# Kernel tuning notes

Hardware: AMD Instinct MI355X
Metric: run time of the kernel (lower is better)

## Reference

```python
import jax, jax.numpy as jnp
import numpy as np


def _propagate(x, src, dst, norm, n):
    # PyG propagate with aggr='add': out[dst_e] += norm_e * x[src_e]
    return jax.ops.segment_sum(x[src] * norm[:, None], dst, num_segments=n)


def _dconv(x, w, b, row, col, norm_out, norm_in, n):
    # DConv with K=2: w has shape (2, 2, c_in, c_out)
    # k=0 term: identity for both diffusion directions
    h = x @ w[0, 0] + x @ w[1, 0]
    # k=1 term: 1-hop diffusion, forward edges and flipped edges
    tx_o = _propagate(x, row, col, norm_out, n)  # out-degree normalized walk
    tx_i = _propagate(x, col, row, norm_in, n)   # edge_index.flip([0]) walk
    h = h + tx_o @ w[0, 1] + tx_i @ w[1, 1]
    return h + b


def reference(x, edge_index, edge_weight, w_lin2, b_lin2, w_z, b_z, w_r, b_r, w_h, b_h, w_out, b_out):
    n = x.shape[0]
    row, col = edge_index[0], edge_index[1]
    # degrees from weighted adjacency (same as to_dense_adj row/col sums)
    deg_out = jax.ops.segment_sum(edge_weight, row, num_segments=n)
    deg_in = jax.ops.segment_sum(edge_weight, col, num_segments=n)
    norm_out = (1.0 / deg_out)[row]
    norm_in = (1.0 / deg_in)[row]

    h = x.reshape(n, -1)                      # Flatten: (n, 24)
    h = jax.nn.sigmoid(h @ w_lin2 + b_lin2)   # (n, hidden)

    # DCRNN GRU cell, hidden state initialized to zeros (single step)
    h0 = jnp.zeros_like(h)
    xh = jnp.concatenate([h, h0], axis=1)     # (n, 2*hidden)
    z = jax.nn.sigmoid(_dconv(xh, w_z, b_z, row, col, norm_out, norm_in, n))
    r = jax.nn.sigmoid(_dconv(xh, w_r, b_r, row, col, norm_out, norm_in, n))
    xhr = jnp.concatenate([h, h0 * r], axis=1)
    h_tilde = jnp.tanh(_dconv(xhr, w_h, b_h, row, col, norm_out, norm_in, n))
    h_new = z * h0 + (1.0 - z) * h_tilde

    return jax.nn.sigmoid(h_new) @ w_out + b_out  # (n, out_periods)


def setup_inputs() -> dict:
    key = jax.random.key(0)
    ks = jax.random.split(key, 12)
    N, DEG, HID, OUTP, WIN, HOR = 100000, 8, 64, 12, 2, 12
    E = N * DEG

    x = jax.random.normal(ks[0], (N, WIN, HOR), dtype=jnp.float32)

    # random edges + a ring so every node has out-degree>=1 and in-degree>=1
    e_rand = N * (DEG - 1)
    row_r = jax.random.randint(ks[1], (e_rand,), 0, N, dtype=jnp.int32)
    col_r = jax.random.randint(ks[2], (e_rand,), 0, N, dtype=jnp.int32)
    ring = jnp.arange(N, dtype=jnp.int32)
    row = jnp.concatenate([row_r, ring])
    col = jnp.concatenate([col_r, (ring + 1) % N])
    edge_index = jnp.stack([row, col])  # (2, E)
    edge_weight = jax.random.uniform(ks[3], (E,), minval=0.5, maxval=1.5, dtype=jnp.float32)

    def lin_w(k, fi, fo):
        return jax.random.normal(k, (fi, fo), jnp.float32) / np.float32(np.sqrt(fi))

    def dconv_w(k, cin, cout):
        return jax.random.normal(k, (2, 2, cin, cout), jnp.float32) / np.float32(np.sqrt(cin))

    cin = 2 * HID
    return {
        "x": x,
        "edge_index": edge_index,
        "edge_weight": edge_weight,
        "w_lin2": lin_w(ks[4], WIN * HOR, HID),
        "b_lin2": jnp.zeros((HID,), jnp.float32),
        "w_z": dconv_w(ks[5], cin, HID),
        "b_z": jnp.zeros((HID,), jnp.float32),
        "w_r": dconv_w(ks[6], cin, HID),
        "b_r": jnp.zeros((HID,), jnp.float32),
        "w_h": dconv_w(ks[7], cin, HID),
        "b_h": jnp.zeros((HID,), jnp.float32),
        "w_out": lin_w(ks[8], HID, OUTP),
        "b_out": jnp.zeros((OUTP,), jnp.float32),
    }
```

## Files before the change

### kernel.cpp

```cpp
#include <hip/hip_runtime.h>


typedef unsigned long long ull;
typedef unsigned short ushort;
typedef unsigned int uint;
typedef __attribute__((ext_vector_type(8))) short bf16x8;
typedef __attribute__((ext_vector_type(4))) float f32x4;

#define BSZ    64
#define CAP    768
#define CHUNK  2048
#define MAXBKT 2048

__device__ __forceinline__ float sigmoid_f(float x) {
    return 1.0f / (1.0f + __expf(-x));
}
__device__ __forceinline__ float tanh_f(float x) {
    float ax = fabsf(x);
    float e = __expf(-2.0f * ax);
    float t = (1.0f - e) / (1.0f + e);
    return copysignf(t, x);
}
__device__ __forceinline__ ushort f2bf(float f) {
    unsigned u = __float_as_uint(f);
    return (ushort)((u + 0x7FFF + ((u >> 16) & 1)) >> 16);
}

__global__ void __launch_bounds__(256) mega1_kernel(
        const int* __restrict__ row, const int* __restrict__ col,
        const float* __restrict__ ew, int E,
        uint* __restrict__ gcur, uint* __restrict__ pkbuf,
        int nbkt, int nslot,
        const float* __restrict__ x, const float* __restrict__ Wl,
        const float* __restrict__ bl, ushort* __restrict__ hb, int N,
        const float* __restrict__ wz, const float* __restrict__ bz,
        const float* __restrict__ wh, const float* __restrict__ bh,
        ushort* __restrict__ Wp, float* __restrict__ bc, int SB, int LB) {
    __shared__ uint smem[MAXBKT];
    int bx = blockIdx.x;
    const int t = threadIdx.x;

    if (bx < SB) {
        uint* hist = smem;
        const int d  = bx & 1;
        const int e0 = (bx >> 1) * CHUNK;
        const int* key = d ? row : col;
        const int* oth = d ? col : row;
        for (int i = t; i < nbkt; i += 256) hist[i] = 0;
        __syncthreads();
#pragma unroll
        for (int j = 0; j < CHUNK / 256; ++j) {
            int e = e0 + j * 256 + t;
            if (e < E) atomicAdd(&hist[key[e] >> 6], 1u);
        }
        __syncthreads();
        for (int i = t; i < nbkt; i += 256) {
            uint c = hist[i];
            hist[i] = c ? (uint)i * CAP + atomicAdd(&gcur[d * nbkt + i], c) : 0u;
        }
        __syncthreads();
#pragma unroll
        for (int j = 0; j < CHUNK / 256; ++j) {
            int e = e0 + j * 256 + t;
            if (e < E) {
                int k   = key[e];
                int bkt = k >> 6;
                uint w9 = (uint)(ew[e] * 256.0f + 0.5f);
                uint s = atomicAdd(&hist[bkt], 1u);
                if (s < ((uint)bkt + 1u) * CAP)
                    pkbuf[(size_t)d * nslot + s] =
                        ((uint)oth[e] << 15) |
                        ((uint)(k & (BSZ - 1)) << 9) | w9;
            }
        }
        return;
    }
    bx -= SB;
    if (bx < LB) {
        float* Ws = (float*)smem;
        float* bs = Ws + 24 * 64;
        for (int i = t; i < 384; i += 256)
            ((float4*)Ws)[i] = ((const float4*)Wl)[i];
        if (t < 64) bs[t] = bl[t];
        __syncthreads();
        const int c = t & 63;
        const int w = t >> 6;
        const int n0 = bx * 16 + w * 4;
#pragma unroll
        for (int q = 0; q < 4; ++q) {
            int n = n0 + q;
            if (n >= N) break;
            const float* xr = x + (size_t)n * 24;
            float acc = bs[c];
#pragma unroll
            for (int k4 = 0; k4 < 6; ++k4) {
                float4 xv = *(const float4*)(xr + k4 * 4);
                acc = fmaf(xv.x, Ws[(k4 * 4 + 0) * 64 + c], acc);
                acc = fmaf(xv.y, Ws[(k4 * 4 + 1) * 64 + c], acc);
                acc = fmaf(xv.z, Ws[(k4 * 4 + 2) * 64 + c], acc);
                acc = fmaf(xv.w, Ws[(k4 * 4 + 3) * 64 + c], acc);
            }
            hb[(size_t)n * 64 + c] = f2bf(sigmoid_f(acc));
        }
        return;
    }
    bx -= LB;
    int i = bx * 256 + t;
    if (bx == 0 && t < 128) bc[t] = (t < 64) ? bz[t] : bh[t - 64];
    if (i >= 6 * 8 * 64 * 8) return;
    int j    = i & 7;
    int lane = (i >> 3) & 63;
    int ct   = (i >> 9) & 7;
    int kt   = i >> 12;
    int k = kt * 32 + 8 * (lane >> 4) + j;
    int c = ct * 16 + (lane & 15);
    const float* w = (c < 64) ? wz : wh;
    int cc = c & 63;
    float v;
    if (k < 64)        v = w[(0 * 128 + k) * 64 + cc] + w[(2 * 128 + k) * 64 + cc];
    else if (k < 128)  v = w[(1 * 128 + (k - 64)) * 64 + cc];
    else               v = w[(3 * 128 + (k - 128)) * 64 + cc];
    Wp[i] = f2bf(v);
}

__global__ void __launch_bounds__(256) sort_kernel(
        const uint* __restrict__ gcur, const uint* __restrict__ pkbuf,
        uint* __restrict__ srt, int2* __restrict__ be,
        float* __restrict__ rdi, float* __restrict__ rdo,
        int nbkt, int nslot, int N) {
    __shared__ uint hist[BSZ];
    __shared__ uint cur[BSZ];
    __shared__ float sdeg[BSZ];
    const int b = blockIdx.x, d = blockIdx.y, t = threadIdx.x;
    if (t < BSZ) { hist[t] = 0; sdeg[t] = 0.0f; }
    __syncthreads();
    uint cnt = gcur[d * nbkt + b];
    if (cnt > CAP) cnt = CAP;
    const uint* rec = pkbuf + (size_t)d * nslot + (size_t)b * CAP;
    for (uint i = t; i < cnt; i += 256) {
        uint r = rec[i];
        uint dl = (r >> 9) & (BSZ - 1);
        atomicAdd(&hist[dl], 1u);
        atomicAdd(&sdeg[dl], (float)(r & 0x1FFu));
    }
    __syncthreads();
    if (t < BSZ) {
        int v = (int)hist[t];
        int x = v;
#pragma unroll
        for (int off = 1; off < BSZ; off <<= 1) {
            int y = __shfl_up(x, off, 64);
            if (t >= off) x += y;
        }
        uint p = (uint)(x - v);
        cur[t] = p;
        int n = b * BSZ + t;
        if (n < N) {
            be[(size_t)d * N + n] =
                make_int2((int)((uint)b * CAP + p),
                          (int)((uint)b * CAP + p + (uint)v));
            float s = sdeg[t];
            float rv = (s > 0.0f) ? (256.0f / s) : 0.0f;
            if (d == 0) rdi[n] = rv;
            else        rdo[n] = rv;
        }
    }
    __syncthreads();
    uint* so = srt + (size_t)d * nslot + (size_t)b * CAP;
    for (uint i = t; i < cnt; i += 256) {
        uint r = rec[i];
        uint dl = (r >> 9) & (BSZ - 1);
        uint p = atomicAdd(&cur[dl], 1u);
        so[p] = r >> 15;
    }
}

__global__ void __launch_bounds__(256) gather_kernel(
        const ushort* __restrict__ hb, const uint* __restrict__ srt,
        const int2* __restrict__ be,
        const float* __restrict__ rdo, const float* __restrict__ rdi,
        ushort* __restrict__ pob, ushort* __restrict__ pib,
        int nslot, int N) {
    const int lane = threadIdx.x & 63;
    const int g    = lane >> 4;
    const int cq   = (lane & 15) * 4;
    const int d    = blockIdx.y;
    const uint* s_  = srt + (size_t)d * nslot;
    const int2* be_ = be + (size_t)d * N;

    int wid  = blockIdx.x * 4 + (threadIdx.x >> 6);
    int step = gridDim.x * 4;
    if (wid >= N) return;

    int2 r0 = be_[wid];
    uint ia = s_[min(r0.x + g,     r0.y - 1)];
    uint ib = s_[min(r0.x + 4 + g, r0.y - 1)];

    for (int n = wid; n < N; n += step) {
        int nn = n + step;
        bool has_next = (nn < N);
        int2 r1 = r0;
        if (has_next) r1 = be_[nn];

        float a0 = 0.f, a1 = 0.f, a2 = 0.f, a3 = 0.f;
        int s = r0.x, e = r0.y;
        while (s < e) {
            int sn = s + 8;
            uint ia_n = ia, ib_n = ib;
            if (sn < e) {
                ia_n = s_[min(sn + g,     e - 1)];
                ib_n = s_[min(sn + 4 + g, e - 1)];
            } else if (has_next) {
                ia_n = s_[min(r1.x + g,     r1.y - 1)];
                ib_n = s_[min(r1.x + 4 + g, r1.y - 1)];
            }
            bool va = (s + g < e), vb = (s + 4 + g < e);
            float wa, wb;
            if (d == 0) {
                wa = va ? rdo[ia] : 0.0f;
                wb = vb ? rdo[ib] : 0.0f;
            } else {
                wa = va ? 1.0f : 0.0f;
                wb = vb ? 1.0f : 0.0f;
            }
            uint2 ha = *(const uint2*)(hb + (size_t)ia * 64 + cq);
            uint2 hc = *(const uint2*)(hb + (size_t)ib * 64 + cq);
            a0 = fmaf(__uint_as_float(ha.x << 16),         wa, a0);
            a1 = fmaf(__uint_as_float(ha.x & 0xFFFF0000u), wa, a1);
            a2 = fmaf(__uint_as_float(ha.y << 16),         wa, a2);
            a3 = fmaf(__uint_as_float(ha.y & 0xFFFF0000u), wa, a3);
            a0 = fmaf(__uint_as_float(hc.x << 16),         wb, a0);
            a1 = fmaf(__uint_as_float(hc.x & 0xFFFF0000u), wb, a1);
            a2 = fmaf(__uint_as_float(hc.y << 16),         wb, a2);
            a3 = fmaf(__uint_as_float(hc.y & 0xFFFF0000u), wb, a3);
            s = sn; ia = ia_n; ib = ib_n;
        }
        a0 += __shfl_xor(a0, 16, 64); a0 += __shfl_xor(a0, 32, 64);
        a1 += __shfl_xor(a1, 16, 64); a1 += __shfl_xor(a1, 32, 64);
        a2 += __shfl_xor(a2, 16, 64); a2 += __shfl_xor(a2, 32, 64);
        a3 += __shfl_xor(a3, 16, 64); a3 += __shfl_xor(a3, 32, 64);

        if (lane < 16) {
            float m = (d == 0) ? 1.0f : rdi[n];
            uint lo = (uint)f2bf(a0 * m) | ((uint)f2bf(a1 * m) << 16);
            uint hi = (uint)f2bf(a2 * m) | ((uint)f2bf(a3 * m) << 16);
            ushort* dst = (d == 0 ? pob : pib) + (size_t)n * 64 + cq;
            *(uint2*)dst = make_uint2(lo, hi);
        }
        r0 = r1;
    }
}

__global__ void __launch_bounds__(256) gates_kernel(
        const ushort* __restrict__ hb, const ushort* __restrict__ pob,
        const ushort* __restrict__ pib, const ushort* __restrict__ Wp,
        const float* __restrict__ bc, const float* __restrict__ wout,
        const float* __restrict__ bout, float* __restrict__ out, int N) {
    __shared__ float sS[64 * 68];
    __shared__ float sWO[64 * 12];
    const int t    = threadIdx.x;
    const int w    = t >> 6;
    const int lane = t & 63;
    const int n0   = blockIdx.x * 64;

    for (int i = t; i < 64 * 12; i += 256) sWO[i] = wout[i];

    f32x4 acc[8];
#pragma unroll
    for (int ct = 0; ct < 8; ++ct) {
        float bcv = bc[ct * 16 + (lane & 15)];
        acc[ct] = (f32x4){bcv, bcv, bcv, bcv};
    }

    int arow = n0 + w * 16 + (lane & 15);
    if (arow >= N) arow = N - 1;
    const int g8 = (lane >> 4) * 8;
    const ushort* const srcs[3] = {hb, pob, pib};

#pragma unroll
    for (int kc = 0; kc < 6; ++kc) {
        const ushort* src = srcs[kc >> 1];
        bf16x8 a = *(const bf16x8*)(src + (size_t)arow * 64 + (kc & 1) * 32 + g8);
#pragma unroll
        for (int ct = 0; ct < 8; ++ct) {
            bf16x8 b = *(const bf16x8*)(Wp + (size_t)((kc * 8 + ct) * 64 + lane) * 8);
            acc[ct] = __builtin_amdgcn_mfma_f32_16x16x32_bf16(a, b, acc[ct], 0, 0, 0);
        }
    }

    const int rowbase = w * 16 + (lane >> 4) * 4;
    const int colbase = lane & 15;
#pragma unroll
    for (int ct = 0; ct < 4; ++ct) {
#pragma unroll
        for (int r = 0; r < 4; ++r) {
            float zv = sigmoid_f(acc[ct][r]);
            float ht = tanh_f(acc[ct + 4][r]);
            sS[(rowbase + r) * 68 + ct * 16 + colbase] =
                sigmoid_f((1.0f - zv) * ht);
        }
    }
    __syncthreads();

#pragma unroll
    for (int rr = 0; rr < 3; ++rr) {
        int o = rr * 256 + t;
        int node = o / 12;
        int j = o % 12;
        int n = n0 + node;
        if (n >= N) continue;
        float a = bout[j];
#pragma unroll 8
        for (int c2 = 0; c2 < 64; ++c2) a = fmaf(sS[node * 68 + c2], sWO[c2 * 12 + j], a);
        out[(size_t)n * 12 + j] = a;
    }
}

extern "C" void kernel_launch(void* const* d_in, const int* in_sizes, int n_in,
                              void* d_out, int out_size, void* d_ws, size_t ws_size,
                              hipStream_t stream) {
    const float* x      = (const float*)d_in[0];
    const int*   ei     = (const int*)  d_in[1];
    const float* ew     = (const float*)d_in[2];
    const float* w_lin2 = (const float*)d_in[3];
    const float* b_lin2 = (const float*)d_in[4];
    const float* w_z    = (const float*)d_in[5];
    const float* b_z    = (const float*)d_in[6];
    const float* w_h    = (const float*)d_in[9];
    const float* b_h    = (const float*)d_in[10];
    const float* w_out  = (const float*)d_in[11];
    const float* b_out  = (const float*)d_in[12];

    int N = in_sizes[0] / 24;
    int E = in_sizes[1] / 2;
    const int* row = ei;
    const int* col = ei + E;
    int nbkt  = (N + BSZ - 1) / BSZ;
    int nslot = nbkt * CAP;

    uint*   pkbuf = (uint*)d_ws;
    uint*   srt   = pkbuf + 2 * (size_t)nslot;
    ushort* hb    = (ushort*)(srt + 2 * (size_t)nslot);
    ushort* pob   = hb  + (size_t)N * 64;
    ushort* pib   = pob + (size_t)N * 64;
    ushort* Wp    = pib + (size_t)N * 64;
    float*  bc    = (float*)(Wp + 24576);
    float*  rdo   = bc + 128;
    float*  rdi   = rdo + N;
    int2*   be    = (int2*)(rdi + N);
    uint*   gcur  = (uint*)(be + 2 * (size_t)N);

    int SB = 2 * ((E + CHUNK - 1) / CHUNK);
    int LB = (N + 15) / 16;
    int PB = (6 * 8 * 64 * 8 + 255) / 256;

    hipMemsetAsync(gcur, 0, 2 * (size_t)nbkt * sizeof(uint), stream);
    mega1_kernel<<<SB + LB + PB, 256, 0, stream>>>(
        row, col, ew, E, gcur, pkbuf, nbkt, nslot,
        x, w_lin2, b_lin2, hb, N,
        w_z, b_z, w_h, b_h, Wp, bc, SB, LB);
    sort_kernel<<<dim3(nbkt, 2), 256, 0, stream>>>(gcur, pkbuf, srt, be,
                                                   rdi, rdo, nbkt, nslot, N);
    gather_kernel<<<dim3(2048, 2), 256, 0, stream>>>(hb, srt, be, rdo, rdi,
                                                     pob, pib, nslot, N);
    gates_kernel<<<(N + 63) / 64, 256, 0, stream>>>(hb, pob, pib, Wp, bc,
                                                    w_out, b_out, (float*)d_out, N);
}
```

Baseline: 151.9 us.

## Fuse bucket sort, neighbor gather and gate GEMM into one per-bucket kernel

Merges the sort, gather and gates kernels into a single kernel that processes one 64-node bucket per block. Sorted edge lists and the propagated features are kept in shared memory instead of being written to and read back from global buffers. A small separate kernel computes the out-degree normalization first, because the gather needs it for source nodes that belong to other buckets. In exchange, each block gathers its own nodes without the prefetch pipelining or the grid-stride load balancing of the old gather kernel, and uses more shared memory per block, which may reduce occupancy.

```diff
diff --git a/kernel.cpp b/kernel.cpp
--- a/kernel.cpp
+++ b/kernel.cpp
@@ -123,171 +123,158 @@
     Wp[i] = f2bf(v);
 }
 
-__global__ void __launch_bounds__(256) sort_kernel(
+__global__ void __launch_bounds__(256) deg1_kernel(
         const uint* __restrict__ gcur, const uint* __restrict__ pkbuf,
-        uint* __restrict__ srt, int2* __restrict__ be,
-        float* __restrict__ rdi, float* __restrict__ rdo,
-        int nbkt, int nslot, int N) {
-    __shared__ uint hist[BSZ];
-    __shared__ uint cur[BSZ];
+        float* __restrict__ rdo, int nbkt, int nslot, int N) {
     __shared__ float sdeg[BSZ];
-    const int b = blockIdx.x, d = blockIdx.y, t = threadIdx.x;
-    if (t < BSZ) { hist[t] = 0; sdeg[t] = 0.0f; }
-    __syncthreads();
-    uint cnt = gcur[d * nbkt + b];
+    const int b = blockIdx.x, t = threadIdx.x;
+    if (t < BSZ) sdeg[t] = 0.0f;
+    __syncthreads();
+    uint cnt = gcur[nbkt + b];
     if (cnt > CAP) cnt = CAP;
-    const uint* rec = pkbuf + (size_t)d * nslot + (size_t)b * CAP;
-    for (uint i = t; i < cnt; i += 256) {
-        uint r = rec[i];
-        uint dl = (r >> 9) & (BSZ - 1);
-        atomicAdd(&hist[dl], 1u);
-        atomicAdd(&sdeg[dl], (float)(r & 0x1FFu));
-    }
+    const uint* rec = pkbuf + (size_t)nslot + (size_t)b * CAP;
+    for (uint i = t; i < cnt; i += 256)
+        atomicAdd(&sdeg[(rec[i] >> 9) & (BSZ - 1)], (float)(rec[i] & 0x1FFu));
     __syncthreads();
     if (t < BSZ) {
-        int v = (int)hist[t];
-        int x = v;
-#pragma unroll
-        for (int off = 1; off < BSZ; off <<= 1) {
-            int y = __shfl_up(x, off, 64);
-            if (t >= off) x += y;
-        }
-        uint p = (uint)(x - v);
-        cur[t] = p;
         int n = b * BSZ + t;
-        if (n < N) {
-            be[(size_t)d * N + n] =
-                make_int2((int)((uint)b * CAP + p),
-                          (int)((uint)b * CAP + p + (uint)v));
-            float s = sdeg[t];
-            float rv = (s > 0.0f) ? (256.0f / s) : 0.0f;
-            if (d == 0) rdi[n] = rv;
-            else        rdo[n] = rv;
-        }
-    }
-    __syncthreads();
-    uint* so = srt + (size_t)d * nslot + (size_t)b * CAP;
-    for (uint i = t; i < cnt; i += 256) {
-        uint r = rec[i];
-        uint dl = (r >> 9) & (BSZ - 1);
-        uint p = atomicAdd(&cur[dl], 1u);
-        so[p] = r >> 15;
-    }
-}
-
-__global__ void __launch_bounds__(256) gather_kernel(
-        const ushort* __restrict__ hb, const uint* __restrict__ srt,
-        const int2* __restrict__ be,
-        const float* __restrict__ rdo, const float* __restrict__ rdi,
-        ushort* __restrict__ pob, ushort* __restrict__ pib,
-        int nslot, int N) {
-    const int lane = threadIdx.x & 63;
-    const int g    = lane >> 4;
-    const int cq   = (lane & 15) * 4;
-    const int d    = blockIdx.y;
-    const uint* s_  = srt + (size_t)d * nslot;
-    const int2* be_ = be + (size_t)d * N;
-
-    int wid  = blockIdx.x * 4 + (threadIdx.x >> 6);
-    int step = gridDim.x * 4;
-    if (wid >= N) return;
-
-    int2 r0 = be_[wid];
-    uint ia = s_[min(r0.x + g,     r0.y - 1)];
-    uint ib = s_[min(r0.x + 4 + g, r0.y - 1)];
-
-    for (int n = wid; n < N; n += step) {
-        int nn = n + step;
-        bool has_next = (nn < N);
-        int2 r1 = r0;
-        if (has_next) r1 = be_[nn];
-
-        float a0 = 0.f, a1 = 0.f, a2 = 0.f, a3 = 0.f;
-        int s = r0.x, e = r0.y;
-        while (s < e) {
-            int sn = s + 8;
-            uint ia_n = ia, ib_n = ib;
-            if (sn < e) {
-                ia_n = s_[min(sn + g,     e - 1)];
-                ib_n = s_[min(sn + 4 + g, e - 1)];
-            } else if (has_next) {
-                ia_n = s_[min(r1.x + g,     r1.y - 1)];
-                ib_n = s_[min(r1.x + 4 + g, r1.y - 1)];
+        if (n < N) rdo[n] = (sdeg[t] > 0.0f) ? (256.0f / sdeg[t]) : 0.0f;
+    }
+}
+
+__global__ void __launch_bounds__(256) mega2_kernel(
+        const uint* __restrict__ gcur, const uint* __restrict__ pkbuf,
+        const ushort* __restrict__ hb, const float* __restrict__ rdo,
+        const ushort* __restrict__ Wp, const float* __restrict__ bc,
+        const float* __restrict__ wout, const float* __restrict__ bout,
+        float* __restrict__ out, int nbkt, int nslot, int N) {
+    __shared__ uint   srt[2][CAP];
+    __shared__ ushort pt[2][BSZ][72];
+    __shared__ uint   histL[BSZ], curL[BSZ];
+    __shared__ uint   begL[2][BSZ];
+    __shared__ ushort cntL[2][BSZ];
+    __shared__ float  sdeg[BSZ], rdi_l[BSZ];
+    __shared__ float  sWO[64 * 12];
+
+    const int b = blockIdx.x, t = threadIdx.x;
+    const int w = t >> 6, lane = t & 63;
+
+    for (int i = t; i < 64 * 12; i += 256) sWO[i] = wout[i];
+
+    for (int d = 0; d < 2; ++d) {
+        if (t < BSZ) { histL[t] = 0; sdeg[t] = 0.0f; }
+        __syncthreads();
+        uint cnt = gcur[d * nbkt + b];
+        if (cnt > CAP) cnt = CAP;
+        const uint* rec = pkbuf + (size_t)d * nslot + (size_t)b * CAP;
+        for (uint i = t; i < cnt; i += 256) {
+            uint r = rec[i];
+            uint dl = (r >> 9) & (BSZ - 1);
+            atomicAdd(&histL[dl], 1u);
+            atomicAdd(&sdeg[dl], (float)(r & 0x1FFu));
+        }
+        __syncthreads();
+        if (t < BSZ) {
+            int v = (int)histL[t];
+            int x = v;
+#pragma unroll
+            for (int off = 1; off < BSZ; off <<= 1) {
+                int y = __shfl_up(x, off, 64);
+                if (t >= off) x += y;
             }
-            bool va = (s + g < e), vb = (s + 4 + g < e);
-            float wa, wb;
-            if (d == 0) {
-                wa = va ? rdo[ia] : 0.0f;
-                wb = vb ? rdo[ib] : 0.0f;
-            } else {
-                wa = va ? 1.0f : 0.0f;
-                wb = vb ? 1.0f : 0.0f;
+            uint p = (uint)(x - v);
+            curL[t] = p;
+            begL[d][t] = p;
+            cntL[d][t] = (ushort)v;
+            if (d == 0) rdi_l[t] = (sdeg[t] > 0.0f) ? (256.0f / sdeg[t]) : 0.0f;
+        }
+        __syncthreads();
+        for (uint i = t; i < cnt; i += 256) {
+            uint r = rec[i];
+            uint dl = (r >> 9) & (BSZ - 1);
+            uint p = atomicAdd(&curL[dl], 1u);
+            srt[d][p] = r >> 15;
+        }
+        __syncthreads();
+    }
+
+    {
+        const int g  = lane >> 4;
+        const int cq = (lane & 15) * 4;
+        for (int d = 0; d < 2; ++d) {
+            for (int nl = w; nl < BSZ; nl += 4) {
+                int s0 = (int)begL[d][nl];
+                int s1 = s0 + (int)cntL[d][nl];
+                float a0 = 0.f, a1 = 0.f, a2 = 0.f, a3 = 0.f;
+                for (int s = s0; s < s1; s += 8) {
+                    int sa = s + g, sb = s + 4 + g;
+                    uint ia = srt[d][(sa < s1) ? sa : s1 - 1];
+                    uint ib = srt[d][(sb < s1) ? sb : s1 - 1];
+                    float wa, wb;
+                    if (d == 0) {
+                        wa = (sa < s1) ? rdo[ia] : 0.0f;
+                        wb = (sb < s1) ? rdo[ib] : 0.0f;
+                    } else {
+                        wa = (sa < s1) ? 1.0f : 0.0f;
+                        wb = (sb < s1) ? 1.0f : 0.0f;
+                    }
+                    uint2 ha = *(const uint2*)(hb + (size_t)ia * 64 + cq);
+                    uint2 hc = *(const uint2*)(hb + (size_t)ib * 64 + cq);
+                    a0 = fmaf(__uint_as_float(ha.x << 16),         wa, a0);
+                    a1 = fmaf(__uint_as_float(ha.x & 0xFFFF0000u), wa, a1);
+                    a2 = fmaf(__uint_as_float(ha.y << 16),         wa, a2);
+                    a3 = fmaf(__uint_as_float(ha.y & 0xFFFF0000u), wa, a3);
+                    a0 = fmaf(__uint_as_float(hc.x << 16),         wb, a0);
+                    a1 = fmaf(__uint_as_float(hc.x & 0xFFFF0000u), wb, a1);
+                    a2 = fmaf(__uint_as_float(hc.y << 16),         wb, a2);
+                    a3 = fmaf(__uint_as_float(hc.y & 0xFFFF0000u), wb, a3);
+                }
+                a0 += __shfl_xor(a0, 16, 64); a0 += __shfl_xor(a0, 32, 64);
+                a1 += __shfl_xor(a1, 16, 64); a1 += __shfl_xor(a1, 32, 64);
+                a2 += __shfl_xor(a2, 16, 64); a2 += __shfl_xor(a2, 32, 64);
+                a3 += __shfl_xor(a3, 16, 64); a3 += __shfl_xor(a3, 32, 64);
+                if (lane < 16) {
+                    float m = (d == 0) ? 1.0f : rdi_l[nl];
+                    uint lo = (uint)f2bf(a0 * m) | ((uint)f2bf(a1 * m) << 16);
+                    uint hi = (uint)f2bf(a2 * m) | ((uint)f2bf(a3 * m) << 16);
+                    *(uint2*)&pt[d][nl][cq] = make_uint2(lo, hi);
+                }
             }
-            uint2 ha = *(const uint2*)(hb + (size_t)ia * 64 + cq);
-            uint2 hc = *(const uint2*)(hb + (size_t)ib * 64 + cq);
-            a0 = fmaf(__uint_as_float(ha.x << 16),         wa, a0);
-            a1 = fmaf(__uint_as_float(ha.x & 0xFFFF0000u), wa, a1);
-            a2 = fmaf(__uint_as_float(ha.y << 16),         wa, a2);
-            a3 = fmaf(__uint_as_float(ha.y & 0xFFFF0000u), wa, a3);
-            a0 = fmaf(__uint_as_float(hc.x << 16),         wb, a0);
-            a1 = fmaf(__uint_as_float(hc.x & 0xFFFF0000u), wb, a1);
-            a2 = fmaf(__uint_as_float(hc.y << 16),         wb, a2);
-            a3 = fmaf(__uint_as_float(hc.y & 0xFFFF0000u), wb, a3);
-            s = sn; ia = ia_n; ib = ib_n;
-        }
-        a0 += __shfl_xor(a0, 16, 64); a0 += __shfl_xor(a0, 32, 64);
-        a1 += __shfl_xor(a1, 16, 64); a1 += __shfl_xor(a1, 32, 64);
-        a2 += __shfl_xor(a2, 16, 64); a2 += __shfl_xor(a2, 32, 64);
-        a3 += __shfl_xor(a3, 16, 64); a3 += __shfl_xor(a3, 32, 64);
-
-        if (lane < 16) {
-            float m = (d == 0) ? 1.0f : rdi[n];
-            uint lo = (uint)f2bf(a0 * m) | ((uint)f2bf(a1 * m) << 16);
-            uint hi = (uint)f2bf(a2 * m) | ((uint)f2bf(a3 * m) << 16);
-            ushort* dst = (d == 0 ? pob : pib) + (size_t)n * 64 + cq;
-            *(uint2*)dst = make_uint2(lo, hi);
-        }
-        r0 = r1;
-    }
-}
-
-__global__ void __launch_bounds__(256) gates_kernel(
-        const ushort* __restrict__ hb, const ushort* __restrict__ pob,
-        const ushort* __restrict__ pib, const ushort* __restrict__ Wp,
-        const float* __restrict__ bc, const float* __restrict__ wout,
-        const float* __restrict__ bout, float* __restrict__ out, int N) {
-    __shared__ float sS[64 * 68];
-    __shared__ float sWO[64 * 12];
-    const int t    = threadIdx.x;
-    const int w    = t >> 6;
-    const int lane = t & 63;
-    const int n0   = blockIdx.x * 64;
-
-    for (int i = t; i < 64 * 12; i += 256) sWO[i] = wout[i];
-
+        }
+    }
+    __syncthreads();
+
+    const int n0 = b * BSZ;
     f32x4 acc[8];
 #pragma unroll
     for (int ct = 0; ct < 8; ++ct) {
         float bcv = bc[ct * 16 + (lane & 15)];
         acc[ct] = (f32x4){bcv, bcv, bcv, bcv};
     }
-
     int arow = n0 + w * 16 + (lane & 15);
     if (arow >= N) arow = N - 1;
     const int g8 = (lane >> 4) * 8;
-    const ushort* const srcs[3] = {hb, pob, pib};
+    const int lrow = w * 16 + (lane & 15);
 
 #pragma unroll
     for (int kc = 0; kc < 6; ++kc) {
-        const ushort* src = srcs[kc >> 1];
-        bf16x8 a = *(const bf16x8*)(src + (size_t)arow * 64 + (kc & 1) * 32 + g8);
+        bf16x8 a;
+        if (kc < 2) {
+            a = *(const bf16x8*)(hb + (size_t)arow * 64 + kc * 32 + g8);
+        } else {
+            const int dd   = (kc - 2) >> 1;
+            const int koff = (kc & 1) * 32;
+            a = *(const bf16x8*)(&pt[dd][lrow][koff + g8]);
+        }
 #pragma unroll
         for (int ct = 0; ct < 8; ++ct) {
-            bf16x8 b = *(const bf16x8*)(Wp + (size_t)((kc * 8 + ct) * 64 + lane) * 8);
-            acc[ct] = __builtin_amdgcn_mfma_f32_16x16x32_bf16(a, b, acc[ct], 0, 0, 0);
-        }
-    }
-
+            bf16x8 bb = *(const bf16x8*)(Wp + (size_t)((kc * 8 + ct) * 64 + lane) * 8);
+            acc[ct] = __builtin_amdgcn_mfma_f32_16x16x32_bf16(a, bb, acc[ct], 0, 0, 0);
+        }
+    }
+
+    __syncthreads();
+    float* sS = (float*)&pt[0][0][0];
     const int rowbase = w * 16 + (lane >> 4) * 4;
     const int colbase = lane & 15;
 #pragma unroll
@@ -311,7 +298,8 @@
         if (n >= N) continue;
         float a = bout[j];
 #pragma unroll 8
-        for (int c2 = 0; c2 < 64; ++c2) a = fmaf(sS[node * 68 + c2], sWO[c2 * 12 + j], a);
+        for (int c2 = 0; c2 < 64; ++c2)
+            a = fmaf(sS[node * 68 + c2], sWO[c2 * 12 + j], a);
         out[(size_t)n * 12 + j] = a;
     }
 }
@@ -339,16 +327,11 @@
     int nslot = nbkt * CAP;
 
     uint*   pkbuf = (uint*)d_ws;
-    uint*   srt   = pkbuf + 2 * (size_t)nslot;
-    ushort* hb    = (ushort*)(srt + 2 * (size_t)nslot);
-    ushort* pob   = hb  + (size_t)N * 64;
-    ushort* pib   = pob + (size_t)N * 64;
-    ushort* Wp    = pib + (size_t)N * 64;
+    ushort* hb    = (ushort*)(pkbuf + 2 * (size_t)nslot);
+    ushort* Wp    = hb + (size_t)N * 64;
     float*  bc    = (float*)(Wp + 24576);
     float*  rdo   = bc + 128;
-    float*  rdi   = rdo + N;
-    int2*   be    = (int2*)(rdi + N);
-    uint*   gcur  = (uint*)(be + 2 * (size_t)N);
+    uint*   gcur  = (uint*)(rdo + N);
 
     int SB = 2 * ((E + CHUNK - 1) / CHUNK);
     int LB = (N + 15) / 16;
@@ -359,10 +342,8 @@
         row, col, ew, E, gcur, pkbuf, nbkt, nslot,
         x, w_lin2, b_lin2, hb, N,
         w_z, b_z, w_h, b_h, Wp, bc, SB, LB);
-    sort_kernel<<<dim3(nbkt, 2), 256, 0, stream>>>(gcur, pkbuf, srt, be,
-                                                   rdi, rdo, nbkt, nslot, N);
-    gather_kernel<<<dim3(2048, 2), 256, 0, stream>>>(hb, srt, be, rdo, rdi,
-                                                     pob, pib, nslot, N);
-    gates_kernel<<<(N + 63) / 64, 256, 0, stream>>>(hb, pob, pib, Wp, bc,
-                                                    w_out, b_out, (float*)d_out, N);
-}
+    deg1_kernel<<<nbkt, 256, 0, stream>>>(gcur, pkbuf, rdo, nbkt, nslot, N);
+    mega2_kernel<<<nbkt, 256, 0, stream>>>(gcur, pkbuf, hb, rdo, Wp, bc,
+                                           w_out, b_out, (float*)d_out,
+                                           nbkt, nslot, N);
+}
```

Measured after the change: 159.1 us. +4.7%, slower.
